# Optimization experiments

Hardware: AMD Instinct MI355X
Metric: run time of the kernel (lower is better)

## Reference

```python
import jax, jax.numpy as jnp
import numpy as np

H = 8          # num heads
D = 16         # head dim
HID = 128      # hidden_dim = H * D
NM, ND, NA = 100000, 20000, 50000
E = 300000     # edges per relation
NUM_CLASSES = 8


def setup_inputs() -> dict:
    key = jax.random.key(0)
    ks = jax.random.split(key, 24)
    s = 0.05
    eye = jnp.eye(D, dtype=jnp.float32)
    inp = {
        'x_movie': jax.random.normal(ks[0], (NM, 256), jnp.float32),
        'x_director': jax.random.normal(ks[1], (ND, 128), jnp.float32),
        'x_actor': jax.random.normal(ks[2], (NA, 128), jnp.float32),
        # edge lists per relation: (director->movie, actor->movie, movie->director, movie->actor)
        'src_dm': jax.random.randint(ks[3], (E,), 0, ND),
        'dst_dm': jax.random.randint(ks[4], (E,), 0, NM),
        'src_am': jax.random.randint(ks[5], (E,), 0, NA),
        'dst_am': jax.random.randint(ks[6], (E,), 0, NM),
        'src_md': jax.random.randint(ks[7], (E,), 0, NM),
        'dst_md': jax.random.randint(ks[8], (E,), 0, ND),
        'src_ma': jax.random.randint(ks[9], (E,), 0, NM),
        'dst_ma': jax.random.randint(ks[10], (E,), 0, NA),
        # per-type pre-encoder (use_pre_encoder=True)
        'Wpre_m': jax.random.normal(ks[11], (256, HID), jnp.float32) * s,
        'Wpre_d': jax.random.normal(ks[12], (128, HID), jnp.float32) * s,
        'Wpre_a': jax.random.normal(ks[13], (128, HID), jnp.float32) * s,
        'bpre': jnp.zeros((3, HID), jnp.float32),
        # per-type K/Q/V projections, stacked over the 3 node types
        'Wk': jax.random.normal(ks[14], (3, HID, HID), jnp.float32) * s,
        'bk': jnp.zeros((3, HID), jnp.float32),
        'Wq': jax.random.normal(ks[15], (3, HID, HID), jnp.float32) * s,
        'bq': jnp.zeros((3, HID), jnp.float32),
        'Wv': jax.random.normal(ks[16], (3, HID, HID), jnp.float32) * s,
        'bv': jnp.zeros((3, HID), jnp.float32),
        # per-relation attention / message matrices and priors (4 relations)
        'a_rel': eye + jax.random.normal(ks[17], (4, H, D, D), jnp.float32) * s,
        'm_rel': eye + jax.random.normal(ks[18], (4, H, D, D), jnp.float32) * s,
        'p_rel': jnp.ones((4, H), jnp.float32),
        # per-type skip gate and output projection
        'skip': jnp.ones((3,), jnp.float32),
        'Wa': jax.random.normal(ks[19], (3, HID, HID), jnp.float32) * s,
        'ba': jnp.zeros((3, HID), jnp.float32),
        # final classification head on target node type ('movie')
        'Wlin': jax.random.normal(ks[20], (HID, NUM_CLASSES), jnp.float32) * s,
        'blin': jnp.zeros((NUM_CLASSES,), jnp.float32),
    }
    return inp


def _seg_softmax_agg(alpha, msg, dst, n):
    # softmax over incoming edges of each destination node, then weighted sum of msgs
    m = jax.ops.segment_max(alpha, dst, num_segments=n)      # [n, H]
    m = jnp.where(jnp.isfinite(m), m, 0.0)
    a = jnp.exp(alpha - m[dst])                              # [E, H]
    denom = jax.ops.segment_sum(a, dst, num_segments=n)      # [n, H]
    num = jax.ops.segment_sum(a[:, :, None] * msg, dst, num_segments=n)  # [n, H, D]
    return num / jnp.maximum(denom, 1e-16)[:, :, None]


def reference(x_movie, x_director, x_actor,
              src_dm, dst_dm, src_am, dst_am, src_md, dst_md, src_ma, dst_ma,
              Wpre_m, Wpre_d, Wpre_a, bpre, Wk, bk, Wq, bq, Wv, bv,
              a_rel, m_rel, p_rel, skip, Wa, ba, Wlin, blin):
    # type order: 0=movie, 1=director, 2=actor
    xs = [x_movie @ Wpre_m + bpre[0],
          x_director @ Wpre_d + bpre[1],
          x_actor @ Wpre_a + bpre[2]]
    k = [(x @ Wk[t] + bk[t]).reshape(-1, H, D) for t, x in enumerate(xs)]
    q = [(x @ Wq[t] + bq[t]).reshape(-1, H, D) for t, x in enumerate(xs)]
    v = [(x @ Wv[t] + bv[t]).reshape(-1, H, D) for t, x in enumerate(xs)]

    # (src_type, dst_type, src_idx, dst_idx) per relation
    rels = [(1, 0, src_dm, dst_dm), (2, 0, src_am, dst_am),
            (0, 1, src_md, dst_md), (0, 2, src_ma, dst_ma)]
    scale = 1.0 / np.sqrt(D).astype(np.float32)
    buckets = {0: [], 1: [], 2: []}
    for r, (st, dt, src, dst) in enumerate(rels):
        ke = jnp.einsum('ehd,hdf->ehf', k[st][src], a_rel[r])          # [E,H,D]
        al = jnp.einsum('ehf,ehf->eh', q[dt][dst], ke) * p_rel[r] * scale
        me = jnp.einsum('ehd,hdf->ehf', v[st][src], m_rel[r])          # [E,H,D]
        buckets[dt].append((al, me, dst))

    n = [x.shape[0] for x in xs]
    outs = []
    for t in range(3):
        al = jnp.concatenate([b[0] for b in buckets[t]], axis=0)
        me = jnp.concatenate([b[1] for b in buckets[t]], axis=0)
        dst = jnp.concatenate([b[2] for b in buckets[t]], axis=0)
        agg = _seg_softmax_agg(al, me, dst, n[t]).reshape(n[t], HID)
        h = jax.nn.gelu(agg, approximate=False) @ Wa[t] + ba[t]
        g = jax.nn.sigmoid(skip[t])
        outs.append(g * h + (1.0 - g) * xs[t])

    return outs[0] @ Wlin + blin
```

## Files before the change

### kernel.cpp

```cpp
#include <hip/hip_runtime.h>
#include <hip/hip_bf16.h>
#include <math.h>

#define NM 100000
#define ND 20000
#define NA 50000
#define EDG 300000
#define CAP 32
#define NBLK_M 782

typedef __attribute__((ext_vector_type(8))) short shortx8;
typedef __attribute__((ext_vector_type(4))) float floatx4;
typedef __attribute__((ext_vector_type(4))) int intx4;

__device__ __forceinline__ float bf2f(unsigned int u) {
    return __uint_as_float(u << 16);
}
__device__ __forceinline__ unsigned short f2bf(float f) {
    unsigned int x = __float_as_uint(f);
    unsigned int r = x + 0x7fffu + ((x >> 16) & 1u);
    return (unsigned short)(r >> 16);
}
__device__ __forceinline__ unsigned short f2bf_fast(float f) {
    return (unsigned short)((__float_as_uint(f) + 0x8000u) >> 16);
}
__device__ __forceinline__ unsigned int pkbf2(float a, float b) {
    return __builtin_amdgcn_perm(__float_as_uint(b) + 0x8000u,
                                 __float_as_uint(a) + 0x8000u,
                                 0x07060302u);
}
__device__ __forceinline__ float gelu_exact(float x) {
    return 0.5f * x * (1.0f + erff(x * 0.70710678118654752f));
}

static const size_t OFF_BT_Q      = 0;
static const size_t OFF_BT_KAMV_D = 73728;
static const size_t OFF_BT_KAMV_A = 139264;
static const size_t OFF_WKA_D     = 204800;
static const size_t OFF_WVM_D     = 270336;
static const size_t OFF_WKA_A     = 335872;
static const size_t OFF_WVM_A     = 401408;
static const size_t OFF_BQ        = 466944;
static const size_t OFF_B_KAMV_D  = 467520;
static const size_t OFF_B_KAMV_A  = 468544;
static const size_t OFF_BKA_D     = 469568;
static const size_t OFF_BVM_D     = 470080;
static const size_t OFF_BKA_A     = 470592;
static const size_t OFF_BVM_A     = 471104;
static const size_t OFF_WALS      = 471616;
static const size_t OFF_BFIN      = 475712;
static const size_t OFF_Q0        = 524288;
static const size_t OFF_SKIPB     = 26124288;
static const size_t OFF_WQT       = 26124288;
static const size_t OFF_KAMV_D    = 29324288;
static const size_t OFF_KAMV_A    = 39564288;
static const size_t OFF_COUNTS    = 65164288;
static const size_t OFF_SLOTS     = 65564288;
#define KAMV_A_DELTA 10240000

__global__ __launch_bounds__(256) void precompA(
    const float* __restrict__ Wk, const float* __restrict__ bk,
    const float* __restrict__ Wv, const float* __restrict__ bv,
    const float* __restrict__ Wa, const float* __restrict__ ba,
    const float* __restrict__ Wlin, const float* __restrict__ blin,
    const float* __restrict__ a_rel, const float* __restrict__ m_rel,
    const float* __restrict__ p_rel, const float* __restrict__ skip,
    const float* __restrict__ bpre, const float* __restrict__ Wq,
    char* __restrict__ ws)
{
    int tid = blockIdx.x * 256 + threadIdx.x;
    if (tid < 65536) {
        int mat = tid >> 14, rem = tid & 16383;
        int e = rem >> 7, hf = rem & 127, h = hf >> 4, f = hf & 15;
        const float* Wsrc; const float* R; float sc; float* dst;
        if (mat == 0)      { Wsrc = Wk + 16384; R = a_rel;        sc = p_rel[h]     * 0.25f; dst = (float*)(ws + OFF_WKA_D); }
        else if (mat == 1) { Wsrc = Wv + 16384; R = m_rel;        sc = 1.0f;                 dst = (float*)(ws + OFF_WVM_D); }
        else if (mat == 2) { Wsrc = Wk + 32768; R = a_rel + 2048; sc = p_rel[8 + h] * 0.25f; dst = (float*)(ws + OFF_WKA_A); }
        else               { Wsrc = Wv + 32768; R = m_rel + 2048; sc = 1.0f;                 dst = (float*)(ws + OFF_WVM_A); }
        float s = 0.0f;
        for (int d = 0; d < 16; d++)
            s += Wsrc[e * 128 + h * 16 + d] * R[h * 256 + d * 16 + f];
        dst[hf * 128 + e] = s * sc;
    } else if (tid < 66048) {
        int idx = tid - 65536;
        int mat = idx >> 7, hf = idx & 127, h = hf >> 4, f = hf & 15;
        const float* bsrc; const float* R; float sc; float* dst;
        if (mat == 0)      { bsrc = bk + 128; R = a_rel;        sc = p_rel[h]     * 0.25f; dst = (float*)(ws + OFF_BKA_D); }
        else if (mat == 1) { bsrc = bv + 128; R = m_rel;        sc = 1.0f;                 dst = (float*)(ws + OFF_BVM_D); }
        else if (mat == 2) { bsrc = bk + 256; R = a_rel + 2048; sc = p_rel[8 + h] * 0.25f; dst = (float*)(ws + OFF_BKA_A); }
        else               { bsrc = bv + 256; R = m_rel + 2048; sc = 1.0f;                 dst = (float*)(ws + OFF_BVM_A); }
        float s = 0.0f;
        for (int d = 0; d < 16; d++)
            s += bsrc[h * 16 + d] * R[h * 256 + d * 16 + f];
        dst[hf] = s * sc;
    } else if (tid < 67072) {
        int idx = tid - 66048;
        int j = idx >> 3, c = idx & 7;
        float g = 1.0f / (1.0f + __expf(-skip[0]));
        float s = 0.0f;
        for (int o = 0; o < 128; o++)
            s += Wa[j * 128 + o] * Wlin[o * 8 + c];
        ((float*)(ws + OFF_WALS))[j * 8 + c] = g * s;
    } else if (tid < 67080) {
        int c = tid - 67072;
        float g = 1.0f / (1.0f + __expf(-skip[0]));
        float s1 = 0.0f, s2 = 0.0f;
        for (int o = 0; o < 128; o++) {
            s1 += ba[o]   * Wlin[o * 8 + c];
            s2 += bpre[o] * Wlin[o * 8 + c];
        }
        ((float*)(ws + OFF_BFIN))[c] = g * s1 + (1.0f - g) * s2 + blin[c];
    } else if (tid < 83464) {
        int i = tid - 67080;
        int n = i >> 7, e = i & 127;
        ((float*)(ws + OFF_WQT))[n * 128 + e] = Wq[e * 128 + n];
    } else if (tid < 83464 + NM) {
        ((int*)(ws + OFF_COUNTS))[tid - 83464] = 0;
    }
}

__device__ __forceinline__ float dot128(const float* __restrict__ a,
                                        const float* __restrict__ b) {
    const floatx4* x = (const floatx4*)a;
    const floatx4* y = (const floatx4*)b;
    float s = 0.0f;
    #pragma unroll
    for (int i = 0; i < 32; i++) {
        floatx4 u = x[i], v = y[i];
        s += u[0] * v[0] + u[1] * v[1] + u[2] * v[2] + u[3] * v[3];
    }
    return s;
}

__global__ __launch_bounds__(256) void prep_scat(
    const int* __restrict__ src_dm, const int* __restrict__ dst_dm,
    const int* __restrict__ src_am, const int* __restrict__ dst_am,
    const float* __restrict__ Wpre_m, const float* __restrict__ Wpre_d,
    const float* __restrict__ Wpre_a, const float* __restrict__ bpre,
    const float* __restrict__ bq, const float* __restrict__ Wlin,
    const float* __restrict__ skip,
    char* __restrict__ ws)
{
    if (blockIdx.x < 2344) {
        int t = blockIdx.x * 256 + threadIdx.x;
        if (t >= 2 * EDG) return;
        int src, dst, delta;
        if (t < EDG) { src = src_dm[t];       dst = dst_dm[t];       delta = 0; }
        else         { src = src_am[t - EDG]; dst = dst_am[t - EDG]; delta = KAMV_A_DELTA; }
        int* counts = (int*)(ws + OFF_COUNTS);
        int* slots  = (int*)(ws + OFF_SLOTS);
        int pos = atomicAdd(&counts[dst], 1);
        if (pos < CAP) slots[(size_t)dst * CAP + pos] = src * 512 + delta;
        return;
    }
    int tid = (blockIdx.x - 2344) * 256 + threadIdx.x;
    const float* WKA_D = (const float*)(ws + OFF_WKA_D);
    const float* WVM_D = (const float*)(ws + OFF_WVM_D);
    const float* WKA_A = (const float*)(ws + OFF_WKA_A);
    const float* WVM_A = (const float*)(ws + OFF_WVM_A);
    const float* WqT   = (const float*)(ws + OFF_WQT);

    if (tid < 36864) {
        int n = tid >> 8, c = tid & 255;
        float s = 0.0f;
        if (n < 128) {
            s = dot128(Wpre_m + c * 128, WqT + n * 128);
        } else if (n < 136) {
            int cc = n - 128;
            float g = 1.0f / (1.0f + __expf(-skip[0]));
            for (int e = 0; e < 128; e++)
                s += Wpre_m[c * 128 + e] * Wlin[e * 8 + cc];
            s *= (1.0f - g);
        }
        ((unsigned short*)(ws + OFF_BT_Q))[n * 256 + c] = f2bf(s);
    } else if (tid < 69632) {
        int idx = tid - 36864;
        int nrow = idx >> 7, c = idx & 127;
        const float* WfT = (nrow < 128) ? WKA_D : WVM_D;
        int nc = nrow & 127;
        float s = dot128(Wpre_d + c * 128, WfT + nc * 128);
        ((unsigned short*)(ws + OFF_BT_KAMV_D))[nrow * 128 + c] = f2bf(s);
    } else if (tid < 102400) {
        int idx = tid - 69632;
        int nrow = idx >> 7, c = idx & 127;
        const float* WfT = (nrow < 128) ? WKA_A : WVM_A;
        int nc = nrow & 127;
        float s = dot128(Wpre_a + c * 128, WfT + nc * 128);
        ((unsigned short*)(ws + OFF_BT_KAMV_A))[nrow * 128 + c] = f2bf(s);
    } else if (tid < 102544) {
        int n = tid - 102400;
        float s = 0.0f;
        if (n < 128) s = dot128(bpre, WqT + n * 128) + bq[n];
        ((float*)(ws + OFF_BQ))[n] = s;
    } else if (tid < 102800) {
        int nrow = tid - 102544;
        const float* WfT = (nrow < 128) ? WKA_D : WVM_D;
        const float* bf_ = (nrow < 128) ? (const float*)(ws + OFF_BKA_D) : (const float*)(ws + OFF_BVM_D);
        int nc = nrow & 127;
        ((float*)(ws + OFF_B_KAMV_D))[nrow] = dot128(bpre + 128, WfT + nc * 128) + bf_[nc];
    } else if (tid < 103056) {
        int nrow = tid - 102800;
        const float* WfT = (nrow < 128) ? WKA_A : WVM_A;
        const float* bf_ = (nrow < 128) ? (const float*)(ws + OFF_BKA_A) : (const float*)(ws + OFF_BVM_A);
        int nc = nrow & 127;
        ((float*)(ws + OFF_B_KAMV_A))[nrow] = dot128(bpre + 256, WfT + nc * 128) + bf_[nc];
    }
}

#define MFMA16(a, b, c) __builtin_amdgcn_mfma_f32_16x16x32_bf16(a, b, c, 0, 0, 0)

__global__ __launch_bounds__(256, 2) void gemm_all(
    const float* __restrict__ xm, const float* __restrict__ xd,
    const float* __restrict__ xa,
    const unsigned short* __restrict__ btq,
    const unsigned short* __restrict__ btd,
    const unsigned short* __restrict__ bta,
    const float* __restrict__ bq,
    const float* __restrict__ bbd, const float* __restrict__ bba,
    unsigned short* __restrict__ q0, float* __restrict__ skipb,
    unsigned short* __restrict__ outd, unsigned short* __restrict__ outa)
{
    __shared__ unsigned short a_lds[128 * 136];
    __shared__ unsigned short b_lds[144 * 136];
    int tid = threadIdx.x;
    int w = tid >> 6, lane = tid & 63;
    int quad = lane >> 4, low = lane & 15;
    int bx = blockIdx.x;

    if (bx < NBLK_M) {
        int row0 = bx * 128;
        floatx4 acc[2][9] = {};
        for (int hfi = 0; hfi < 2; hfi++) {
            if (hfi) __syncthreads();
            intx4 bvv[9];
            #pragma unroll
            for (int it = 0; it < 9; it++) {
                int idx = it * 256 + tid, n = idx >> 4, ch = idx & 15;
                bvv[it] = *(const intx4*)&btq[(size_t)n * 256 + hfi * 128 + ch * 8];
            }
            floatx4 av[16];
            #pragma unroll
            for (int it = 0; it < 16; it++) {
                int f = it * 256 + tid, r = f >> 5, c4 = f & 31;
                int rg = row0 + r; if (rg >= NM) rg = NM - 1;
                av[it] = *(const floatx4*)(xm + (size_t)rg * 256 + hfi * 128 + c4 * 4);
            }
            #pragma unroll
            for (int it = 0; it < 9; it++) {
                int idx = it * 256 + tid, n = idx >> 4, ch = idx & 15;
                *(intx4*)&b_lds[n * 136 + ch * 8] = bvv[it];
            }
            #pragma unroll
            for (int it = 0; it < 16; it++) {
                int f = it * 256 + tid, r = f >> 5, c4 = f & 31;
                unsigned long long d =
                    ((unsigned long long)pkbf2(av[it][2], av[it][3]) << 32) |
                    pkbf2(av[it][0], av[it][1]);
                *(unsigned long long*)&a_lds[r * 136 + c4 * 4] = d;
            }
            __syncthreads();
            #pragma unroll
            for (int ks = 0; ks < 4; ks++) {
                int ko = ks * 32 + quad * 8;
                shortx8 a0 = *(const shortx8*)&a_lds[(w * 32 + low) * 136 + ko];
                shortx8 a1 = *(const shortx8*)&a_lds[(w * 32 + 16 + low) * 136 + ko];
                #pragma unroll
                for (int nt = 0; nt < 9; nt++) {
                    shortx8 b = *(const shortx8*)&b_lds[(nt * 16 + low) * 136 + ko];
                    acc[0][nt] = MFMA16(a0, b, acc[0][nt]);
                    acc[1][nt] = MFMA16(a1, b, acc[1][nt]);
                }
            }
        }
        int rb = row0 + w * 32;
        #pragma unroll
        for (int mt = 0; mt < 2; mt++) {
            #pragma unroll
            for (int nt = 0; nt < 9; nt++) {
                #pragma unroll
                for (int r = 0; r < 4; r++) {
                    int row = rb + mt * 16 + quad * 4 + r;
                    if (row >= NM) continue;
                    int col = nt * 16 + low;
                    float v = acc[mt][nt][r] + bq[col];
                    if (nt == 8) {
                        if (low < 8) skipb[(size_t)row * 8 + low] = v;
                    } else {
                        q0[(size_t)row * 128 + col] = f2bf_fast(v);
                    }
                }
            }
        }
    } else {
        int rem = bx - NBLK_M;
        const float* A; const unsigned short* BT; const float* bias;
        unsigned short* outb; int M, kbx, cofs;
        if (rem < 157)      { A = xd; BT = btd;             bias = bbd;       outb = outd; M = ND; kbx = rem;       cofs = 0;   }
        else if (rem < 314) { A = xd; BT = btd + 128 * 128; bias = bbd + 128; outb = outd; M = ND; kbx = rem - 157; cofs = 128; }
        else if (rem < 705) { A = xa; BT = bta;             bias = bba;       outb = outa; M = NA; kbx = rem - 314; cofs = 0;   }
        else                { A = xa; BT = bta + 128 * 128; bias = bba + 128; outb = outa; M = NA; kbx = rem - 705; cofs = 128; }
        int row0 = kbx * 128;

        intx4 bvv[8];
        #pragma unroll
        for (int it = 0; it < 8; it++) {
            int idx = it * 256 + tid, n = idx >> 4, ch = idx & 15;
            bvv[it] = *(const intx4*)&BT[(size_t)n * 128 + ch * 8];
        }
        floatx4 av[16];
        #pragma unroll
        for (int it = 0; it < 16; it++) {
            int f = it * 256 + tid, r = f >> 5, c4 = f & 31;
            int rg = row0 + r; if (rg >= M) rg = M - 1;
            av[it] = *(const floatx4*)(A + (size_t)rg * 128 + c4 * 4);
        }
        #pragma unroll
        for (int it = 0; it < 8; it++) {
            int idx = it * 256 + tid, n = idx >> 4, ch = idx & 15;
            *(intx4*)&b_lds[n * 136 + ch * 8] = bvv[it];
        }
        #pragma unroll
        for (int it = 0; it < 16; it++) {
            int f = it * 256 + tid, r = f >> 5, c4 = f & 31;
            unsigned long long d =
                ((unsigned long long)pkbf2(av[it][2], av[it][3]) << 32) |
                pkbf2(av[it][0], av[it][1]);
            *(unsigned long long*)&a_lds[r * 136 + c4 * 4] = d;
        }
        __syncthreads();

        floatx4 acc[2][8] = {};
        #pragma unroll
        for (int ks = 0; ks < 4; ks++) {
            int ko = ks * 32 + quad * 8;
            shortx8 a0 = *(const shortx8*)&a_lds[(w * 32 + low) * 136 + ko];
            shortx8 a1 = *(const shortx8*)&a_lds[(w * 32 + 16 + low) * 136 + ko];
            #pragma unroll
            for (int nt = 0; nt < 8; nt++) {
                shortx8 b = *(const shortx8*)&b_lds[(nt * 16 + low) * 136 + ko];
                acc[0][nt] = MFMA16(a0, b, acc[0][nt]);
                acc[1][nt] = MFMA16(a1, b, acc[1][nt]);
            }
        }
        int rb = row0 + w * 32;
        #pragma unroll
        for (int mt = 0; mt < 2; mt++) {
            #pragma unroll
            for (int nt = 0; nt < 8; nt++) {
                #pragma unroll
                for (int r = 0; r < 4; r++) {
                    int row = rb + mt * 16 + quad * 4 + r;
                    if (row >= M) continue;
                    int col = nt * 16 + low;
                    outb[(size_t)row * 256 + cofs + col] = f2bf_fast(acc[mt][nt][r] + bias[col]);
                }
            }
        }
    }
}

__global__ __launch_bounds__(256) void agg_kernel(
    const unsigned short* __restrict__ q0,
    const char* __restrict__ kamv0,
    const int* __restrict__ counts, const int* __restrict__ slots,
    const float* __restrict__ skipb,
    const float* __restrict__ WaLs, const float* __restrict__ bfin,
    float* __restrict__ out)
{
    __shared__ float wals[1032];
    for (int i = threadIdx.x; i < 1024; i += 256) {
        int c = i >> 7, rem = i & 127, j = rem >> 4, L = rem & 15;
        wals[i] = WaLs[(L * 8 + j) * 8 + c];
    }
    if (threadIdx.x < 8) wals[1024 + threadIdx.x] = bfin[threadIdx.x];
    __syncthreads();

    int lane = threadIdx.x & 63;
    int grp = lane >> 4;
    int L   = lane & 15;
    int n = blockIdx.x * 16 + (threadIdx.x >> 6) * 4 + grp;

    intx4 qv = *(const intx4*)(q0 + (size_t)n * 128 + L * 8);
    float qf[8];
    #pragma unroll
    for (int d = 0; d < 4; d++) {
        unsigned int u = (unsigned int)qv[d];
        qf[2 * d]     = __uint_as_float(u << 16);
        qf[2 * d + 1] = __uint_as_float(u & 0xffff0000u);
    }

    int cnt = counts[n];
    cnt = cnt < 0 ? 0 : (cnt > CAP ? CAP : cnt);
    int s0 = slots[(size_t)n * CAP + L];

    float acc[8] = {0, 0, 0, 0, 0, 0, 0, 0};
    float den = 0.0f;
    for (int i = 0; i < cnt; i++) {
        int off = __shfl(s0, (lane & 48) + (i & 15));
        if (__builtin_expect(i >= 16, 0)) off = slots[(size_t)n * CAP + i];
        const char* p = kamv0 + off;
        intx4 ku = *(const intx4*)(p + L * 16);
        intx4 mu = *(const intx4*)(p + 256 + L * 16);
        float ph = 0.0f;
        #pragma unroll
        for (int d = 0; d < 4; d++) {
            unsigned int u = (unsigned int)ku[d];
            ph += qf[2 * d]     * __uint_as_float(u << 16);
            ph += qf[2 * d + 1] * __uint_as_float(u & 0xffff0000u);
        }
        float pf = ph + __shfl_xor(ph, 1);
        float wgt = __expf(fminf(pf, 60.0f));
        den += wgt;
        #pragma unroll
        for (int d = 0; d < 4; d++) {
            unsigned int u = (unsigned int)mu[d];
            acc[2 * d]     += wgt * __uint_as_float(u << 16);
            acc[2 * d + 1] += wgt * __uint_as_float(u & 0xffff0000u);
        }
    }
    float inv = 1.0f / fmaxf(den, 1e-16f);

    float part[8] = {0, 0, 0, 0, 0, 0, 0, 0};
    #pragma unroll
    for (int j = 0; j < 8; j++) {
        float u = gelu_exact(acc[j] * inv);
        #pragma unroll
        for (int c = 0; c < 8; c++)
            part[c] += u * wals[c * 128 + j * 16 + L];
    }

    bool b0 = lane & 1, b1 = lane & 2, b2 = lane & 4;
    float t1[4], t2[2], t3;
    #pragma unroll
    for (int k = 0; k < 4; k++) {
        float send = b0 ? part[k] : part[4 + k];
        float got  = __shfl_xor(send, 1);
        t1[k] = (b0 ? part[4 + k] : part[k]) + got;
    }
    #pragma unroll
    for (int k = 0; k < 2; k++) {
        float send = b1 ? t1[k] : t1[2 + k];
        float got  = __shfl_xor(send, 2);
        t2[k] = (b1 ? t1[2 + k] : t1[k]) + got;
    }
    {
        float send = b2 ? t2[0] : t2[1];
        float got  = __shfl_xor(send, 4);
        t3 = (b2 ? t2[1] : t2[0]) + got;
    }
    t3 += __shfl_xor(t3, 8);
    if (L < 8) {
        int c = 4 * (L & 1) + 2 * ((L >> 1) & 1) + ((L >> 2) & 1);
        out[(size_t)n * 8 + c] = t3 + skipb[(size_t)n * 8 + c] + wals[1024 + c];
    }
}

extern "C" void kernel_launch(void* const* d_in, const int* in_sizes, int n_in,
                              void* d_out, int out_size, void* d_ws, size_t ws_size,
                              hipStream_t stream) {
    (void)in_sizes; (void)n_in; (void)out_size; (void)ws_size;
    const float* x_movie    = (const float*)d_in[0];
    const float* x_director = (const float*)d_in[1];
    const float* x_actor    = (const float*)d_in[2];
    const int* src_dm = (const int*)d_in[3];
    const int* dst_dm = (const int*)d_in[4];
    const int* src_am = (const int*)d_in[5];
    const int* dst_am = (const int*)d_in[6];
    const float* Wpre_m = (const float*)d_in[11];
    const float* Wpre_d = (const float*)d_in[12];
    const float* Wpre_a = (const float*)d_in[13];
    const float* bpre   = (const float*)d_in[14];
    const float* Wk     = (const float*)d_in[15];
    const float* bk     = (const float*)d_in[16];
    const float* Wq     = (const float*)d_in[17];
    const float* bq     = (const float*)d_in[18];
    const float* Wv     = (const float*)d_in[19];
    const float* bv     = (const float*)d_in[20];
    const float* a_rel  = (const float*)d_in[21];
    const float* m_rel  = (const float*)d_in[22];
    const float* p_rel  = (const float*)d_in[23];
    const float* skip   = (const float*)d_in[24];
    const float* Wa     = (const float*)d_in[25];
    const float* ba     = (const float*)d_in[26];
    const float* Wlin   = (const float*)d_in[27];
    const float* blin   = (const float*)d_in[28];

    char* ws = (char*)d_ws;
    float* out = (float*)d_out;

    precompA<<<(83464 + NM + 255) / 256, 256, 0, stream>>>(
        Wk, bk, Wv, bv, Wa, ba, Wlin, blin,
        a_rel, m_rel, p_rel, skip, bpre, Wq, ws);

    prep_scat<<<2344 + 403, 256, 0, stream>>>(
        src_dm, dst_dm, src_am, dst_am,
        Wpre_m, Wpre_d, Wpre_a, bpre, bq, Wlin, skip, ws);

    gemm_all<<<NBLK_M + 1096, 256, 0, stream>>>(
        x_movie, x_director, x_actor,
        (const unsigned short*)(ws + OFF_BT_Q),
        (const unsigned short*)(ws + OFF_BT_KAMV_D),
        (const unsigned short*)(ws + OFF_BT_KAMV_A),
        (const float*)(ws + OFF_BQ),
        (const float*)(ws + OFF_B_KAMV_D), (const float*)(ws + OFF_B_KAMV_A),
        (unsigned short*)(ws + OFF_Q0), (float*)(ws + OFF_SKIPB),
        (unsigned short*)(ws + OFF_KAMV_D), (unsigned short*)(ws + OFF_KAMV_A));

    agg_kernel<<<NM / 16, 256, 0, stream>>>(
        (const unsigned short*)(ws + OFF_Q0),
        (const char*)(ws + OFF_KAMV_D),
        (const int*)(ws + OFF_COUNTS), (const int*)(ws + OFF_SLOTS),
        (const float*)(ws + OFF_SKIPB),
        (const float*)(ws + OFF_WALS), (const float*)(ws + OFF_BFIN), out);
}
```

Before: 398.4 us.

## Halve GEMM row tiles, prefetch second K-half, and software-pipeline aggregation gathers

The fused GEMM kernel now uses 64-row tiles instead of 128, which doubles the block count and halves LDS A usage. It also issues the global loads for the second K-half (movie) or second output half (director/actor) before the first MFMA pass, so those loads overlap with compute. The Q weight buffer is re-laid out into two contiguous 128-column halves to support this. In the aggregation kernel, the K/V gather for the next edge is issued before the current edge is computed. Together these aim to hide memory latency and improve occupancy, at the cost of more register pressure and extra B-tile reloads per block.

```diff
diff --git a/kernel.cpp b/kernel.cpp
--- a/kernel.cpp
+++ b/kernel.cpp
@@ -7,7 +7,9 @@
 #define NA 50000
 #define EDG 300000
 #define CAP 32
-#define NBLK_M 782
+#define NBLK_M 1563
+#define NBLK_D 313
+#define NBLK_A 782
 
 typedef __attribute__((ext_vector_type(8))) short shortx8;
 typedef __attribute__((ext_vector_type(4))) float floatx4;
@@ -172,7 +174,7 @@
                 s += Wpre_m[c * 128 + e] * Wlin[e * 8 + cc];
             s *= (1.0f - g);
         }
-        ((unsigned short*)(ws + OFF_BT_Q))[n * 256 + c] = f2bf(s);
+        ((unsigned short*)(ws + OFF_BT_Q))[(c >> 7) * 18432 + n * 128 + (c & 127)] = f2bf(s);
     } else if (tid < 69632) {
         int idx = tid - 36864;
         int nrow = idx >> 7, c = idx & 127;
@@ -220,7 +222,7 @@
     unsigned short* __restrict__ q0, float* __restrict__ skipb,
     unsigned short* __restrict__ outd, unsigned short* __restrict__ outa)
 {
-    __shared__ unsigned short a_lds[128 * 136];
+    __shared__ unsigned short a_lds[64 * 136];
     __shared__ unsigned short b_lds[144 * 136];
     int tid = threadIdx.x;
     int w = tid >> 6, lane = tid & 63;
@@ -228,99 +230,27 @@
     int bx = blockIdx.x;
 
     if (bx < NBLK_M) {
-        int row0 = bx * 128;
-        floatx4 acc[2][9] = {};
-        for (int hfi = 0; hfi < 2; hfi++) {
-            if (hfi) __syncthreads();
-            intx4 bvv[9];
-            #pragma unroll
-            for (int it = 0; it < 9; it++) {
-                int idx = it * 256 + tid, n = idx >> 4, ch = idx & 15;
-                bvv[it] = *(const intx4*)&btq[(size_t)n * 256 + hfi * 128 + ch * 8];
-            }
-            floatx4 av[16];
-            #pragma unroll
-            for (int it = 0; it < 16; it++) {
-                int f = it * 256 + tid, r = f >> 5, c4 = f & 31;
-                int rg = row0 + r; if (rg >= NM) rg = NM - 1;
-                av[it] = *(const floatx4*)(xm + (size_t)rg * 256 + hfi * 128 + c4 * 4);
-            }
-            #pragma unroll
-            for (int it = 0; it < 9; it++) {
-                int idx = it * 256 + tid, n = idx >> 4, ch = idx & 15;
-                *(intx4*)&b_lds[n * 136 + ch * 8] = bvv[it];
-            }
-            #pragma unroll
-            for (int it = 0; it < 16; it++) {
-                int f = it * 256 + tid, r = f >> 5, c4 = f & 31;
-                unsigned long long d =
-                    ((unsigned long long)pkbf2(av[it][2], av[it][3]) << 32) |
-                    pkbf2(av[it][0], av[it][1]);
-                *(unsigned long long*)&a_lds[r * 136 + c4 * 4] = d;
-            }
-            __syncthreads();
-            #pragma unroll
-            for (int ks = 0; ks < 4; ks++) {
-                int ko = ks * 32 + quad * 8;
-                shortx8 a0 = *(const shortx8*)&a_lds[(w * 32 + low) * 136 + ko];
-                shortx8 a1 = *(const shortx8*)&a_lds[(w * 32 + 16 + low) * 136 + ko];
-                #pragma unroll
-                for (int nt = 0; nt < 9; nt++) {
-                    shortx8 b = *(const shortx8*)&b_lds[(nt * 16 + low) * 136 + ko];
-                    acc[0][nt] = MFMA16(a0, b, acc[0][nt]);
-                    acc[1][nt] = MFMA16(a1, b, acc[1][nt]);
-                }
-            }
-        }
-        int rb = row0 + w * 32;
-        #pragma unroll
-        for (int mt = 0; mt < 2; mt++) {
-            #pragma unroll
-            for (int nt = 0; nt < 9; nt++) {
-                #pragma unroll
-                for (int r = 0; r < 4; r++) {
-                    int row = rb + mt * 16 + quad * 4 + r;
-                    if (row >= NM) continue;
-                    int col = nt * 16 + low;
-                    float v = acc[mt][nt][r] + bq[col];
-                    if (nt == 8) {
-                        if (low < 8) skipb[(size_t)row * 8 + low] = v;
-                    } else {
-                        q0[(size_t)row * 128 + col] = f2bf_fast(v);
-                    }
-                }
-            }
-        }
-    } else {
-        int rem = bx - NBLK_M;
-        const float* A; const unsigned short* BT; const float* bias;
-        unsigned short* outb; int M, kbx, cofs;
-        if (rem < 157)      { A = xd; BT = btd;             bias = bbd;       outb = outd; M = ND; kbx = rem;       cofs = 0;   }
-        else if (rem < 314) { A = xd; BT = btd + 128 * 128; bias = bbd + 128; outb = outd; M = ND; kbx = rem - 157; cofs = 128; }
-        else if (rem < 705) { A = xa; BT = bta;             bias = bba;       outb = outa; M = NA; kbx = rem - 314; cofs = 0;   }
-        else                { A = xa; BT = bta + 128 * 128; bias = bba + 128; outb = outa; M = NA; kbx = rem - 705; cofs = 128; }
-        int row0 = kbx * 128;
-
-        intx4 bvv[8];
-        #pragma unroll
-        for (int it = 0; it < 8; it++) {
-            int idx = it * 256 + tid, n = idx >> 4, ch = idx & 15;
-            bvv[it] = *(const intx4*)&BT[(size_t)n * 128 + ch * 8];
-        }
-        floatx4 av[16];
-        #pragma unroll
-        for (int it = 0; it < 16; it++) {
+        int row0 = bx * 64;
+        intx4 bv[9];
+        #pragma unroll
+        for (int it = 0; it < 9; it++) {
+            int idx = it * 256 + tid, n = idx >> 4, ch = idx & 15;
+            bv[it] = *(const intx4*)&btq[(size_t)n * 128 + ch * 8];
+        }
+        floatx4 av[8];
+        #pragma unroll
+        for (int it = 0; it < 8; it++) {
             int f = it * 256 + tid, r = f >> 5, c4 = f & 31;
-            int rg = row0 + r; if (rg >= M) rg = M - 1;
-            av[it] = *(const floatx4*)(A + (size_t)rg * 128 + c4 * 4);
-        }
-        #pragma unroll
-        for (int it = 0; it < 8; it++) {
-            int idx = it * 256 + tid, n = idx >> 4, ch = idx & 15;
-            *(intx4*)&b_lds[n * 136 + ch * 8] = bvv[it];
-        }
-        #pragma unroll
-        for (int it = 0; it < 16; it++) {
+            int rg = row0 + r; if (rg >= NM) rg = NM - 1;
+            av[it] = *(const floatx4*)(xm + (size_t)rg * 256 + c4 * 4);
+        }
+        #pragma unroll
+        for (int it = 0; it < 9; it++) {
+            int idx = it * 256 + tid, n = idx >> 4, ch = idx & 15;
+            *(intx4*)&b_lds[n * 136 + ch * 8] = bv[it];
+        }
+        #pragma unroll
+        for (int it = 0; it < 8; it++) {
             int f = it * 256 + tid, r = f >> 5, c4 = f & 31;
             unsigned long long d =
                 ((unsigned long long)pkbf2(av[it][2], av[it][3]) << 32) |
@@ -329,30 +259,167 @@
         }
         __syncthreads();
 
-        floatx4 acc[2][8] = {};
+        intx4 bv1[9];
+        #pragma unroll
+        for (int it = 0; it < 9; it++) {
+            int idx = it * 256 + tid, n = idx >> 4, ch = idx & 15;
+            bv1[it] = *(const intx4*)&btq[18432 + (size_t)n * 128 + ch * 8];
+        }
+        floatx4 av1[8];
+        #pragma unroll
+        for (int it = 0; it < 8; it++) {
+            int f = it * 256 + tid, r = f >> 5, c4 = f & 31;
+            int rg = row0 + r; if (rg >= NM) rg = NM - 1;
+            av1[it] = *(const floatx4*)(xm + (size_t)rg * 256 + 128 + c4 * 4);
+        }
+
+        floatx4 acc[9] = {};
         #pragma unroll
         for (int ks = 0; ks < 4; ks++) {
             int ko = ks * 32 + quad * 8;
-            shortx8 a0 = *(const shortx8*)&a_lds[(w * 32 + low) * 136 + ko];
-            shortx8 a1 = *(const shortx8*)&a_lds[(w * 32 + 16 + low) * 136 + ko];
-            #pragma unroll
-            for (int nt = 0; nt < 8; nt++) {
+            shortx8 a0 = *(const shortx8*)&a_lds[(w * 16 + low) * 136 + ko];
+            #pragma unroll
+            for (int nt = 0; nt < 9; nt++) {
                 shortx8 b = *(const shortx8*)&b_lds[(nt * 16 + low) * 136 + ko];
-                acc[0][nt] = MFMA16(a0, b, acc[0][nt]);
-                acc[1][nt] = MFMA16(a1, b, acc[1][nt]);
-            }
-        }
-        int rb = row0 + w * 32;
-        #pragma unroll
-        for (int mt = 0; mt < 2; mt++) {
+                acc[nt] = MFMA16(a0, b, acc[nt]);
+            }
+        }
+        __syncthreads();
+        #pragma unroll
+        for (int it = 0; it < 9; it++) {
+            int idx = it * 256 + tid, n = idx >> 4, ch = idx & 15;
+            *(intx4*)&b_lds[n * 136 + ch * 8] = bv1[it];
+        }
+        #pragma unroll
+        for (int it = 0; it < 8; it++) {
+            int f = it * 256 + tid, r = f >> 5, c4 = f & 31;
+            unsigned long long d =
+                ((unsigned long long)pkbf2(av1[it][2], av1[it][3]) << 32) |
+                pkbf2(av1[it][0], av1[it][1]);
+            *(unsigned long long*)&a_lds[r * 136 + c4 * 4] = d;
+        }
+        __syncthreads();
+        #pragma unroll
+        for (int ks = 0; ks < 4; ks++) {
+            int ko = ks * 32 + quad * 8;
+            shortx8 a0 = *(const shortx8*)&a_lds[(w * 16 + low) * 136 + ko];
+            #pragma unroll
+            for (int nt = 0; nt < 9; nt++) {
+                shortx8 b = *(const shortx8*)&b_lds[(nt * 16 + low) * 136 + ko];
+                acc[nt] = MFMA16(a0, b, acc[nt]);
+            }
+        }
+
+        int rb = row0 + w * 16;
+        #pragma unroll
+        for (int nt = 0; nt < 9; nt++) {
+            #pragma unroll
+            for (int r = 0; r < 4; r++) {
+                int row = rb + quad * 4 + r;
+                if (row >= NM) continue;
+                int col = nt * 16 + low;
+                float v = acc[nt][r] + bq[col];
+                if (nt == 8) {
+                    if (low < 8) skipb[(size_t)row * 8 + low] = v;
+                } else {
+                    q0[(size_t)row * 128 + col] = f2bf_fast(v);
+                }
+            }
+        }
+    } else {
+        int rem = bx - NBLK_M;
+        const float* A; const unsigned short* BT; const float* bias;
+        unsigned short* outb; int M, kbx;
+        if (rem < NBLK_D) { A = xd; BT = btd; bias = bbd; outb = outd; M = ND; kbx = rem; }
+        else              { A = xa; BT = bta; bias = bba; outb = outa; M = NA; kbx = rem - NBLK_D; }
+        int row0 = kbx * 64;
+
+        intx4 bv[8];
+        #pragma unroll
+        for (int it = 0; it < 8; it++) {
+            int idx = it * 256 + tid, n = idx >> 4, ch = idx & 15;
+            bv[it] = *(const intx4*)&BT[(size_t)n * 128 + ch * 8];
+        }
+        floatx4 av[8];
+        #pragma unroll
+        for (int it = 0; it < 8; it++) {
+            int f = it * 256 + tid, r = f >> 5, c4 = f & 31;
+            int rg = row0 + r; if (rg >= M) rg = M - 1;
+            av[it] = *(const floatx4*)(A + (size_t)rg * 128 + c4 * 4);
+        }
+        #pragma unroll
+        for (int it = 0; it < 8; it++) {
+            int idx = it * 256 + tid, n = idx >> 4, ch = idx & 15;
+            *(intx4*)&b_lds[n * 136 + ch * 8] = bv[it];
+        }
+        #pragma unroll
+        for (int it = 0; it < 8; it++) {
+            int f = it * 256 + tid, r = f >> 5, c4 = f & 31;
+            unsigned long long d =
+                ((unsigned long long)pkbf2(av[it][2], av[it][3]) << 32) |
+                pkbf2(av[it][0], av[it][1]);
+            *(unsigned long long*)&a_lds[r * 136 + c4 * 4] = d;
+        }
+        __syncthreads();
+
+        intx4 bv1[8];
+        #pragma unroll
+        for (int it = 0; it < 8; it++) {
+            int idx = it * 256 + tid, n = idx >> 4, ch = idx & 15;
+            bv1[it] = *(const intx4*)&BT[16384 + (size_t)n * 128 + ch * 8];
+        }
+
+        int rb = row0 + w * 16;
+        {
+            floatx4 acc[8] = {};
+            #pragma unroll
+            for (int ks = 0; ks < 4; ks++) {
+                int ko = ks * 32 + quad * 8;
+                shortx8 a0 = *(const shortx8*)&a_lds[(w * 16 + low) * 136 + ko];
+                #pragma unroll
+                for (int nt = 0; nt < 8; nt++) {
+                    shortx8 b = *(const shortx8*)&b_lds[(nt * 16 + low) * 136 + ko];
+                    acc[nt] = MFMA16(a0, b, acc[nt]);
+                }
+            }
             #pragma unroll
             for (int nt = 0; nt < 8; nt++) {
                 #pragma unroll
                 for (int r = 0; r < 4; r++) {
-                    int row = rb + mt * 16 + quad * 4 + r;
+                    int row = rb + quad * 4 + r;
                     if (row >= M) continue;
                     int col = nt * 16 + low;
-                    outb[(size_t)row * 256 + cofs + col] = f2bf_fast(acc[mt][nt][r] + bias[col]);
+                    outb[(size_t)row * 256 + col] = f2bf_fast(acc[nt][r] + bias[col]);
+                }
+            }
+        }
+        __syncthreads();
+        #pragma unroll
+        for (int it = 0; it < 8; it++) {
+            int idx = it * 256 + tid, n = idx >> 4, ch = idx & 15;
+            *(intx4*)&b_lds[n * 136 + ch * 8] = bv1[it];
+        }
+        __syncthreads();
+        {
+            floatx4 acc[8] = {};
+            #pragma unroll
+            for (int ks = 0; ks < 4; ks++) {
+                int ko = ks * 32 + quad * 8;
+                shortx8 a0 = *(const shortx8*)&a_lds[(w * 16 + low) * 136 + ko];
+                #pragma unroll
+                for (int nt = 0; nt < 8; nt++) {
+                    shortx8 b = *(const shortx8*)&b_lds[(nt * 16 + low) * 136 + ko];
+                    acc[nt] = MFMA16(a0, b, acc[nt]);
+                }
+            }
+            #pragma unroll
+            for (int nt = 0; nt < 8; nt++) {
+                #pragma unroll
+                for (int r = 0; r < 4; r++) {
+                    int row = rb + quad * 4 + r;
+                    if (row >= M) continue;
+                    int col = nt * 16 + low;
+                    outb[(size_t)row * 256 + 128 + col] = f2bf_fast(acc[nt][r] + bias[128 + col]);
                 }
             }
         }
@@ -395,27 +462,36 @@
 
     float acc[8] = {0, 0, 0, 0, 0, 0, 0, 0};
     float den = 0.0f;
-    for (int i = 0; i < cnt; i++) {
-        int off = __shfl(s0, (lane & 48) + (i & 15));
-        if (__builtin_expect(i >= 16, 0)) off = slots[(size_t)n * CAP + i];
-        const char* p = kamv0 + off;
+    if (cnt > 0) {
+        int off0 = __shfl(s0, lane & 48);
+        const char* p = kamv0 + off0;
         intx4 ku = *(const intx4*)(p + L * 16);
         intx4 mu = *(const intx4*)(p + 256 + L * 16);
-        float ph = 0.0f;
-        #pragma unroll
-        for (int d = 0; d < 4; d++) {
-            unsigned int u = (unsigned int)ku[d];
-            ph += qf[2 * d]     * __uint_as_float(u << 16);
-            ph += qf[2 * d + 1] * __uint_as_float(u & 0xffff0000u);
-        }
-        float pf = ph + __shfl_xor(ph, 1);
-        float wgt = __expf(fminf(pf, 60.0f));
-        den += wgt;
-        #pragma unroll
-        for (int d = 0; d < 4; d++) {
-            unsigned int u = (unsigned int)mu[d];
-            acc[2 * d]     += wgt * __uint_as_float(u << 16);
-            acc[2 * d + 1] += wgt * __uint_as_float(u & 0xffff0000u);
+        for (int i = 0; i < cnt; i++) {
+            int inext = (i + 1 < cnt) ? i + 1 : i;
+            int offn = __shfl(s0, (lane & 48) + (inext & 15));
+            if (__builtin_expect(inext >= 16, 0)) offn = slots[(size_t)n * CAP + inext];
+            const char* pn = kamv0 + offn;
+            intx4 kun = *(const intx4*)(pn + L * 16);
+            intx4 mun = *(const intx4*)(pn + 256 + L * 16);
+
+            float ph = 0.0f;
+            #pragma unroll
+            for (int d = 0; d < 4; d++) {
+                unsigned int u = (unsigned int)ku[d];
+                ph += qf[2 * d]     * __uint_as_float(u << 16);
+                ph += qf[2 * d + 1] * __uint_as_float(u & 0xffff0000u);
+            }
+            float pf = ph + __shfl_xor(ph, 1);
+            float wgt = __expf(fminf(pf, 60.0f));
+            den += wgt;
+            #pragma unroll
+            for (int d = 0; d < 4; d++) {
+                unsigned int u = (unsigned int)mu[d];
+                acc[2 * d]     += wgt * __uint_as_float(u << 16);
+                acc[2 * d + 1] += wgt * __uint_as_float(u & 0xffff0000u);
+            }
+            ku = kun; mu = mun;
         }
     }
     float inv = 1.0f / fmaxf(den, 1e-16f);
@@ -496,7 +572,7 @@
         src_dm, dst_dm, src_am, dst_am,
         Wpre_m, Wpre_d, Wpre_a, bpre, bq, Wlin, skip, ws);
 
-    gemm_all<<<NBLK_M + 1096, 256, 0, stream>>>(
+    gemm_all<<<NBLK_M + NBLK_D + NBLK_A, 256, 0, stream>>>(
         x_movie, x_director, x_actor,
         (const unsigned short*)(ws + OFF_BT_Q),
         (const unsigned short*)(ws + OFF_BT_KAMV_D),
```

Result: no change. 396.0 us (-0.6%).
